# Performance work log

Measured on AMD Instinct MI355X. Metric: run time of the kernel, lower is better.

The kernel has to match this reference:

```python
import jax, jax.numpy as jnp
import numpy as np

B, S, D, H, F, L = 16, 512, 512, 8, 2048, 3  # L layers: 1 in blocks_1 + 2 in blocks_2
DK = D // H
EPS = 1e-5

def setup_inputs():
    key = jax.random.key(0)
    ks = jax.random.split(key, 10)
    sc = 1.0 / np.sqrt(D)
    return dict(
        q_embed_data=jax.random.normal(ks[0], (B, S, D), jnp.float32),
        qa_embed_data=jax.random.normal(ks[1], (B, S, D), jnp.float32),
        Wk=jax.random.normal(ks[2], (L, D, D), jnp.float32) * sc,
        bk=jnp.zeros((L, D), jnp.float32),
        Wv=jax.random.normal(ks[3], (L, D, D), jnp.float32) * sc,
        bv=jnp.zeros((L, D), jnp.float32),
        Wo=jax.random.normal(ks[4], (L, D, D), jnp.float32) * sc,
        bo=jnp.zeros((L, D), jnp.float32),
        gammas=jax.random.normal(ks[5], (L, H, 1, 1), jnp.float32) * 0.5,
        ln1_g=jnp.ones((L, D), jnp.float32),
        ln1_b=jnp.zeros((L, D), jnp.float32),
        W1=jax.random.normal(ks[6], (L, D, F), jnp.float32) * sc,
        b1=jnp.zeros((L, F), jnp.float32),
        W2=jax.random.normal(ks[7], (L, F, D), jnp.float32) * (1.0 / np.sqrt(F)),
        b2=jnp.zeros((L, D), jnp.float32),
        ln2_g=jnp.ones((L, D), jnp.float32),
        ln2_b=jnp.zeros((L, D), jnp.float32),
    )

def _ln(x, g, b):
    m = jnp.mean(x, -1, keepdims=True)
    v = jnp.mean((x - m) ** 2, -1, keepdims=True)
    return (x - m) * jax.lax.rsqrt(v + EPS) * g + b

def _attention(q, k, v, mask, gamma):
    # q,k,v: [B,H,S,DK]; mask: [1,1,S,S] bool; gamma: [H,1,1]
    scores = jnp.einsum('bhid,bhjd->bhij', q, k) / np.sqrt(DK)
    maskf = mask.astype(scores.dtype)
    # first (no-grad in torch) softmax pass for distance decay
    p = jax.nn.softmax(jnp.where(mask, scores, -1e32), axis=-1) * maskf
    distcum = jnp.cumsum(p, axis=-1)
    disttot = jnp.sum(p, axis=-1, keepdims=True)
    idx = jnp.arange(scores.shape[-1])
    pos = jnp.abs(idx[None, :] - idx[:, None]).astype(scores.dtype)[None, None]
    dist = jax.lax.stop_gradient(
        jnp.sqrt(jnp.clip((disttot - distcum) * pos, 0.0, None)))
    g = -jax.nn.softplus(gamma)[None]  # [1,H,1,1]
    total_effect = jnp.clip(jnp.exp(dist * g), 1e-5, 1e5)
    scores = jnp.where(mask, scores * total_effect, -1e32)
    attn = jax.nn.softmax(scores, axis=-1)
    return jnp.einsum('bhij,bhjd->bhid', attn, v)

def _mha(q_in, k_in, v_in, mask, Wk, bk, Wv, bv, Wo, bo, gamma):
    bsz = q_in.shape[0]
    def proj(x, W, b):
        return (x @ W + b).reshape(bsz, -1, H, DK).transpose(0, 2, 1, 3)
    q = proj(q_in, Wk, bk)  # kq_same=True -> q uses k_linear
    k = proj(k_in, Wk, bk)
    v = proj(v_in, Wv, bv)
    o = _attention(q, k, v, mask, gamma)
    o = o.transpose(0, 2, 1, 3).reshape(bsz, -1, D)
    return o @ Wo + bo

def _block(i, mask, query, key, values, apply_pos, P):
    q2 = _mha(query, key, values, mask, P['Wk'][i], P['bk'][i], P['Wv'][i],
              P['bv'][i], P['Wo'][i], P['bo'][i], P['gammas'][i])
    x = _ln(query + q2, P['ln1_g'][i], P['ln1_b'][i])
    if apply_pos:
        h = jax.nn.relu(x @ P['W1'][i] + P['b1'][i]) @ P['W2'][i] + P['b2'][i]
        x = _ln(x + h, P['ln2_g'][i], P['ln2_b'][i])
    return x

def reference(q_embed_data, qa_embed_data, Wk, bk, Wv, bv, Wo, bo, gammas,
              ln1_g, ln1_b, W1, b1, W2, b2, ln2_g, ln2_b):
    P = dict(Wk=Wk, bk=bk, Wv=Wv, bv=bv, Wo=Wo, bo=bo, gammas=gammas,
             ln1_g=ln1_g, ln1_b=ln1_b, W1=W1, b1=b1, W2=W2, b2=b2,
             ln2_g=ln2_g, ln2_b=ln2_b)
    s = q_embed_data.shape[1]
    mask1 = jnp.tril(jnp.ones((s, s), bool))[None, None]        # mask==1: current+past
    mask0 = jnp.tril(jnp.ones((s, s), bool), -1)[None, None]    # mask==0: strictly past
    y = qa_embed_data
    x = q_embed_data
    y = _block(0, mask1, y, y, y, True, P)    # blocks_1: knowledge encoder
    x = _block(1, mask1, x, x, x, False, P)   # blocks_2: question encoder (no FFN)
    x = _block(2, mask0, x, x, y, True, P)    # blocks_2: knowledge retriever
    return x
```

## Files before the change

### kernel.cpp

```cpp
#include <hip/hip_runtime.h>
#include <hip/hip_bf16.h>

#define Bdim 16
#define Sdim 512
#define Ddim 512
#define Hdim 8
#define DKdim 64
#define Fdim 2048
#define Mrows (Bdim * Sdim)

typedef __attribute__((ext_vector_type(8))) short  frag16;
typedef __attribute__((ext_vector_type(4))) float  f32x4;
typedef __attribute__((ext_vector_type(8))) unsigned short ushort8;
typedef __attribute__((ext_vector_type(4))) unsigned short ushort4v;

__device__ __forceinline__ unsigned short f2b(float x) {
    union { float f; unsigned int u; } v; v.f = x;
    unsigned int r = (v.u + 0x7FFFu + ((v.u >> 16) & 1u)) >> 16;
    return (unsigned short)r;
}

__global__ __launch_bounds__(256) void gemm_mfma(
    const __hip_bfloat16* __restrict__ A, const __hip_bfloat16* __restrict__ Bt,
    const float* __restrict__ bias, const float* __restrict__ R,
    float* __restrict__ Cf, unsigned short* __restrict__ Cb,
    int M, int N, int K, int do_relu)
{
    __shared__ short As[2][128 * 32];
    __shared__ short Bs[2][128 * 32];

    const int t = threadIdx.x;
    const int lane = t & 63;
    const int wave = t >> 6;

    const int gx = gridDim.x;
    const int nb = gx * gridDim.y;
    const int lid = blockIdx.x + gx * blockIdx.y;
    const int wid = (lid & 7) * (nb >> 3) + (lid >> 3);
    const int bm = (wid / gx) * 128;
    const int bn = (wid % gx) * 128;

    const int wm = (wave >> 1) * 64;
    const int wn = (wave & 1) * 64;

    f32x4 acc[4][4] = {};
    const int lrow = lane >> 2;
    const int lcol = (lane & 3) * 8;

    auto stage = [&](int k0, int buf) {
#pragma unroll
        for (int i = 0; i < 2; ++i) {
            const int chunk = wave * 2 + i;
            const int row = chunk * 16 + lrow;
            const __hip_bfloat16* ga = A + (size_t)(bm + row) * K + k0 + lcol;
            const __hip_bfloat16* gb = Bt + (size_t)(bn + row) * K + k0 + lcol;
            __builtin_amdgcn_global_load_lds(
                (const __attribute__((address_space(1))) unsigned int*)ga,
                (__attribute__((address_space(3))) unsigned int*)(&As[buf][chunk * 512]),
                16, 0, 0);
            __builtin_amdgcn_global_load_lds(
                (const __attribute__((address_space(1))) unsigned int*)gb,
                (__attribute__((address_space(3))) unsigned int*)(&Bs[buf][chunk * 512]),
                16, 0, 0);
        }
    };

    const int fr = lane & 15;
    const int quad = lane >> 4;
    const int nk = K >> 5;

    stage(0, 0);
    __syncthreads();

    for (int it = 0; it < nk; ++it) {
        const int buf = it & 1;
        if (it + 1 < nk) stage((it + 1) << 5, buf ^ 1);
        frag16 af[4], bfr[4];
#pragma unroll
        for (int i = 0; i < 4; ++i) {
            af[i]  = *(const frag16*)(&As[buf][(wm + i * 16 + fr) * 32 + quad * 8]);
            bfr[i] = *(const frag16*)(&Bs[buf][(wn + i * 16 + fr) * 32 + quad * 8]);
        }
#pragma unroll
        for (int mi = 0; mi < 4; ++mi)
#pragma unroll
            for (int ni = 0; ni < 4; ++ni)
                acc[mi][ni] = __builtin_amdgcn_mfma_f32_16x16x32_bf16(
                    af[mi], bfr[ni], acc[mi][ni], 0, 0, 0);
        __syncthreads();
    }

#pragma unroll
    for (int mi = 0; mi < 4; ++mi) {
#pragma unroll
        for (int r = 0; r < 4; ++r) {
            const int m = bm + wm + mi * 16 + quad * 4 + r;
#pragma unroll
            for (int ni = 0; ni < 4; ++ni) {
                const int n = bn + wn + ni * 16 + fr;
                float v = acc[mi][ni][r] + bias[n];
                if (R) v += R[(size_t)m * N + n];
                if (do_relu) v = fmaxf(v, 0.f);
                if (Cf) Cf[(size_t)m * N + n] = v;
                if (Cb) Cb[(size_t)m * N + n] = f2b(v);
            }
        }
    }
}

__global__ __launch_bounds__(256) void gemm_n64(
    const unsigned short* __restrict__ A0, const unsigned short* __restrict__ A1,
    const unsigned short* __restrict__ B0, const unsigned short* __restrict__ B1,
    const float* __restrict__ bias0, const float* __restrict__ bias1,
    const float* __restrict__ R, float* __restrict__ Cf,
    unsigned short* __restrict__ Cb, unsigned short* __restrict__ CbT,
    int K)
{
    const int NN = 512;
    __shared__ short As[2][128 * 32];
    __shared__ short Bs[2][64 * 32];

    const int trans = blockIdx.z;
    const unsigned short* A  = trans ? A1 : A0;
    const unsigned short* Bt = trans ? B1 : B0;
    const float* bias        = trans ? bias1 : bias0;

    const int t = threadIdx.x;
    const int lane = t & 63;
    const int wave = t >> 6;

    const int lid = blockIdx.x + 8 * blockIdx.y;
    const int wid = (lid & 7) * 64 + (lid >> 3);
    const int bm = (wid >> 3) * 128;
    const int bn = (wid & 7) * 64;

    const int wm = (wave >> 1) * 64;
    const int wn = (wave & 1) * 32;

    f32x4 acc[4][2] = {};
    const int lrow = lane >> 2;
    const int lcol = (lane & 3) * 8;

    auto stage = [&](int k0, int buf) {
#pragma unroll
        for (int i = 0; i < 2; ++i) {
            const int chunk = wave * 2 + i;
            const int row = chunk * 16 + lrow;
            const unsigned short* ga = A + (size_t)(bm + row) * K + k0 + lcol;
            __builtin_amdgcn_global_load_lds(
                (const __attribute__((address_space(1))) unsigned int*)ga,
                (__attribute__((address_space(3))) unsigned int*)(&As[buf][chunk * 512]),
                16, 0, 0);
        }
        {
            const int row = wave * 16 + lrow;
            const unsigned short* gb = Bt + (size_t)(bn + row) * K + k0 + lcol;
            __builtin_amdgcn_global_load_lds(
                (const __attribute__((address_space(1))) unsigned int*)gb,
                (__attribute__((address_space(3))) unsigned int*)(&Bs[buf][wave * 512]),
                16, 0, 0);
        }
    };

    const int fr = lane & 15;
    const int quad = lane >> 4;
    const int nk = K >> 5;

    stage(0, 0);
    __syncthreads();

    for (int it = 0; it < nk; ++it) {
        const int buf = it & 1;
        if (it + 1 < nk) stage((it + 1) << 5, buf ^ 1);
        frag16 af[4], bfr[2];
#pragma unroll
        for (int i = 0; i < 4; ++i)
            af[i] = *(const frag16*)(&As[buf][(wm + i * 16 + fr) * 32 + quad * 8]);
#pragma unroll
        for (int i = 0; i < 2; ++i)
            bfr[i] = *(const frag16*)(&Bs[buf][(wn + i * 16 + fr) * 32 + quad * 8]);
#pragma unroll
        for (int mi = 0; mi < 4; ++mi)
#pragma unroll
            for (int ni = 0; ni < 2; ++ni)
                acc[mi][ni] = __builtin_amdgcn_mfma_f32_16x16x32_bf16(
                    af[mi], bfr[ni], acc[mi][ni], 0, 0, 0);
        __syncthreads();
    }

    if (trans) {
#pragma unroll
        for (int mi = 0; mi < 4; ++mi)
#pragma unroll
            for (int ni = 0; ni < 2; ++ni) {
                const int m = bm + wm + mi * 16 + quad * 4;
                const int n = bn + wn + ni * 16 + fr;
                ushort4v o;
#pragma unroll
                for (int r = 0; r < 4; ++r) o[r] = f2b(acc[mi][ni][r] + bias[n]);
                const int bb = m >> 9, s = m & 511;
                const int hh = n >> 6, dd = n & 63;
                *(ushort4v*)(CbT + (((size_t)((bb * Hdim + hh) * DKdim + dd)) << 9) + s) = o;
            }
        return;
    }

#pragma unroll
    for (int mi = 0; mi < 4; ++mi) {
#pragma unroll
        for (int r = 0; r < 4; ++r) {
            const int m = bm + wm + mi * 16 + quad * 4 + r;
#pragma unroll
            for (int ni = 0; ni < 2; ++ni) {
                const int n = bn + wn + ni * 16 + fr;
                float v = acc[mi][ni][r] + bias[n];
                if (R) v += R[(size_t)m * NN + n];
                if (Cf) Cf[(size_t)m * NN + n] = v;
                if (Cb) Cb[(size_t)m * NN + n] = f2b(v);
            }
        }
    }
}

__global__ __launch_bounds__(256) void conv_b(
    const float* __restrict__ X, unsigned short* __restrict__ Y)
{
    const size_t i = ((size_t)blockIdx.x * 256 + threadIdx.x) * 8;
    float4 a = *(const float4*)(X + i);
    float4 b = *(const float4*)(X + i + 4);
    ushort8 o;
    o[0] = f2b(a.x); o[1] = f2b(a.y); o[2] = f2b(a.z); o[3] = f2b(a.w);
    o[4] = f2b(b.x); o[5] = f2b(b.y); o[6] = f2b(b.z); o[7] = f2b(b.w);
    *(ushort8*)(Y + i) = o;
}

__global__ __launch_bounds__(256) void wtrans_all(
    const float* __restrict__ Wk, const float* __restrict__ Wv,
    const float* __restrict__ Wo, const float* __restrict__ W1,
    const float* __restrict__ W2, unsigned short* __restrict__ dst)
{
    const int bid = blockIdx.x;
    const float* src; unsigned short* d; int K, N, tk, tn;
    if (bid < 576) {
        const int mat = bid >> 6, tile = bid & 63;
        const int l = mat / 3, wch = mat % 3;
        const float* W = (wch == 0) ? Wk : (wch == 1) ? Wv : Wo;
        src = W + (size_t)l * 262144;
        d = dst + (size_t)mat * 262144;
        K = 512; N = 512; tn = tile & 7; tk = tile >> 3;
    } else if (bid < 1088) {
        const int idx = bid - 576, l2 = idx >> 8, tile = idx & 255;
        src = W1 + (size_t)(l2 * 2) * (512 * 2048);
        d = dst + 9 * 262144 + (size_t)l2 * (512 * 2048);
        K = 512; N = 2048; tn = tile & 31; tk = tile >> 5;
    } else {
        const int idx = bid - 1088, l2 = idx >> 8, tile = idx & 255;
        src = W2 + (size_t)(l2 * 2) * (2048 * 512);
        d = dst + 9 * 262144 + 2 * (512 * 2048) + (size_t)l2 * (2048 * 512);
        K = 2048; N = 512; tn = tile & 7; tk = tile >> 3;
    }
    const int n0 = tn * 64, k0 = tk * 64;
    __shared__ float T[64][65];
    const int t = threadIdx.x;
    const int kl = t >> 4, n4 = (t & 15) << 2;
#pragma unroll
    for (int it = 0; it < 4; ++it) {
        const int k = kl + it * 16;
        float4 v = *(const float4*)(src + (size_t)(k0 + k) * N + n0 + n4);
        T[n4 + 0][k] = v.x; T[n4 + 1][k] = v.y;
        T[n4 + 2][k] = v.z; T[n4 + 3][k] = v.w;
    }
    __syncthreads();
    const int nl = t >> 3, k8 = (t & 7) << 3;
#pragma unroll
    for (int it = 0; it < 2; ++it) {
        const int n = nl + it * 32;
        ushort8 o;
#pragma unroll
        for (int c = 0; c < 8; ++c) o[c] = f2b(T[n][k8 + c]);
        *(ushort8*)(d + (size_t)(n0 + n) * K + k0 + k8) = o;
    }
}

__global__ __launch_bounds__(128, 16) void attn_flash6(
    const unsigned short* __restrict__ Kb,
    const unsigned short* __restrict__ Vt,
    const float* __restrict__ gam,
    unsigned short* __restrict__ Ob,
    int mask_type)
{
    __shared__ float CTw[16 * 33];
    __shared__ unsigned short Pst[2][16 * 36];
    __shared__ float S1s[2][16];
    __shared__ float S2s[2][16];
    __shared__ float OaccS[16 * 66];

    const int h = blockIdx.y, b = blockIdx.z;
    const int tile = (blockIdx.x + blockIdx.y + 2 * blockIdx.z) & 31;

    const int t = threadIdx.x, lane = t & 63, p = t >> 6;
    const int quad = lane >> 4, fr = lane & 15;
    const int q0 = tile * 16;
    const int iRow = q0 + fr;

    const unsigned short* kbase = Kb + (size_t)b * Sdim * Ddim + h * DKdim;

    frag16 aq0 = *(const frag16*)(kbase + (size_t)(q0 + fr) * Ddim + quad * 8);
    frag16 aq1 = *(const frag16*)(kbase + (size_t)(q0 + fr) * Ddim + 32 + quad * 8);

    const int jnmax = tile;

    float psum = 0.f;
    for (int jn = p; jn <= jnmax; jn += 2) {
        frag16 k0 = *(const frag16*)(kbase + (size_t)(jn * 16 + fr) * Ddim + quad * 8);
        frag16 k1 = *(const frag16*)(kbase + (size_t)(jn * 16 + fr) * Ddim + 32 + quad * 8);
        f32x4 z = {0.f, 0.f, 0.f, 0.f};
        z = __builtin_amdgcn_mfma_f32_16x16x32_bf16(k0, aq0, z, 0, 0, 0);
        z = __builtin_amdgcn_mfma_f32_16x16x32_bf16(k1, aq1, z, 0, 0, 0);
        const int jbase = jn * 16 + quad * 4;
        float tq = 0.f;
#pragma unroll
        for (int r = 0; r < 4; ++r) {
            const int j = jbase + r;
            const bool valid = mask_type ? (j <= iRow) : (j < iRow);
            tq += valid ? __expf(z[r] * 0.125f) : 0.f;
        }
        psum += tq;
        float tt = tq;
        tt += __shfl_xor(tt, 16);
        tt += __shfl_xor(tt, 32);
        if (quad == 0) CTw[fr * 33 + jn] = tt;
    }
    {
        float s1 = psum;
        s1 += __shfl_xor(s1, 16);
        s1 += __shfl_xor(s1, 32);
        if (lane < 16) S1s[p][lane] = s1;
    }
    __syncthreads();

    if (p == 0 && lane < 16) {
        float run = 0.f;
        for (int jn = 31; jn >= 0; --jn) {
            const float tv = (jn <= jnmax) ? CTw[lane * 33 + jn] : 0.f;
            CTw[lane * 33 + jn] = run;
            run += tv;
        }
    }
    __syncthreads();

    const float rsum1 = 1.f / (S1s[0][fr] + S1s[1][fr]);
    const float gneg = -log1pf(__expf(gam[h]));

    unsigned short* Pw = Pst[p];
    const unsigned short* vtb = Vt + (size_t)(b * Hdim + h) * DKdim * Sdim;
    const bool fm_blk = (mask_type == 0) && (q0 == 0);
    const bool fmrow = (mask_type == 0) && (iRow == 0);
    const int umax = fm_blk ? (Sdim / 32 - 1) : (tile >> 1);
    float sum2p = 0.f;
    f32x4 oacc[4] = {};

    for (int u = umax - p; u >= 0; u -= 2) {
#pragma unroll
        for (int half = 0; half < 2; ++half) {
            const int jn = 2 * u + half;
            frag16 k0 = *(const frag16*)(kbase + (size_t)(jn * 16 + fr) * Ddim + quad * 8);
            frag16 k1 = *(const frag16*)(kbase + (size_t)(jn * 16 + fr) * Ddim + 32 + quad * 8);
            f32x4 z = {0.f, 0.f, 0.f, 0.f};
            z = __builtin_amdgcn_mfma_f32_16x16x32_bf16(k0, aq0, z, 0, 0, 0);
            z = __builtin_amdgcn_mfma_f32_16x16x32_bf16(k1, aq1, z, 0, 0, 0);
            const int jbase = jn * 16 + quad * 4;
            float s[4], e1[4], lsuf[4];
            float tq = 0.f;
#pragma unroll
            for (int r = 3; r >= 0; --r) {
                lsuf[r] = tq;
                const int j = jbase + r;
                const bool valid = mask_type ? (j <= iRow) : (j < iRow);
                s[r] = z[r] * 0.125f;
                e1[r] = valid ? __expf(s[r]) : 0.f;
                tq += e1[r];
            }
            float incl = tq;
            {
                float u1 = __shfl_down(incl, 16);
                incl += (quad < 3) ? u1 : 0.f;
                float u2 = __shfl_down(incl, 32);
                incl += (quad < 2) ? u2 : 0.f;
            }
            const float qsuf = incl - tq;
            const float ct = CTw[fr * 33 + jn];
            ushort4v pk;
#pragma unroll
            for (int r = 0; r < 4; ++r) {
                const int j = jbase + r;
                const bool valid = mask_type ? (j <= iRow) : (j < iRow);
                const float suf = ct + qsuf + lsuf[r];
                const float ratio = suf * rsum1;
                const int dd = iRow - j;
                const float pos = (float)(dd >= 0 ? dd : -dd);
                const float arg = (ratio > 0.f) ? ratio * pos : 0.f;
                const float te = fminf(fmaxf(__expf(gneg * sqrtf(arg)), 1e-5f), 1e5f);
                const float e2 = valid ? __expf(s[r] * te) : (fmrow ? 1.f : 0.f);
                sum2p += e2;
                pk[r] = f2b(e2);
            }
            *(ushort4v*)(Pw + fr * 36 + half * 16 + quad * 4) = pk;
        }
        frag16 pf = *(const frag16*)(Pw + fr * 36 + quad * 8);
        const int jb = u * 32;
#pragma unroll
        for (int dt = 0; dt < 4; ++dt) {
            frag16 vf = *(const frag16*)(vtb + (size_t)(dt * 16 + fr) * Sdim + jb + quad * 8);
            oacc[dt] = __builtin_amdgcn_mfma_f32_16x16x32_bf16(pf, vf, oacc[dt], 0, 0, 0);
        }
    }

    {
        float s2 = sum2p;
        s2 += __shfl_xor(s2, 16);
        s2 += __shfl_xor(s2, 32);
        if (lane < 16) S2s[p][lane] = s2;
    }
    if (p == 1) {
#pragma unroll
        for (int dt = 0; dt < 4; ++dt)
#pragma unroll
            for (int r = 0; r < 4; ++r)
                OaccS[(quad * 4 + r) * 66 + dt * 16 + fr] = oacc[dt][r];
    }
    __syncthreads();

    if (p == 0) {
        const float rs2 = 1.f / (S2s[0][fr] + S2s[1][fr]);
        float rs2q[4];
#pragma unroll
        for (int r = 0; r < 4; ++r) rs2q[r] = __shfl(rs2, quad * 4 + r);

        unsigned short* obase = Ob + ((size_t)(b * Sdim + q0)) * Ddim + h * DKdim;
#pragma unroll
        for (int dt = 0; dt < 4; ++dt)
#pragma unroll
            for (int r = 0; r < 4; ++r) {
                const float v = oacc[dt][r] + OaccS[(quad * 4 + r) * 66 + dt * 16 + fr];
                obase[(size_t)(quad * 4 + r) * Ddim + dt * 16 + fr] = f2b(v * rs2q[r]);
            }
    }
}

__global__ __launch_bounds__(256) void ln_kernel(
    const float* __restrict__ X, const float* __restrict__ g,
    const float* __restrict__ bta, float* __restrict__ Y,
    unsigned short* __restrict__ Yb)
{
    const int row = blockIdx.x;
    const int t = threadIdx.x;
    __shared__ float r1[256], r2[256];
    const float* x = X + (size_t)row * Ddim;
    float a = x[t], b = x[t + 256];
    r1[t] = a + b;
    r2[t] = a * a + b * b;
    __syncthreads();
    for (int off = 128; off; off >>= 1) {
        if (t < off) { r1[t] += r1[t + off]; r2[t] += r2[t + off]; }
        __syncthreads();
    }
    float mean = r1[0] * (1.f / Ddim);
    float var = r2[0] * (1.f / Ddim) - mean * mean;
    float rs = rsqrtf(var + 1e-5f);
    float y0 = (a - mean) * rs * g[t] + bta[t];
    float y1 = (b - mean) * rs * g[t + 256] + bta[t + 256];
    if (Y) {
        float* y = Y + (size_t)row * Ddim;
        y[t] = y0;
        y[t + 256] = y1;
    }
    if (Yb) {
        unsigned short* yb = Yb + (size_t)row * Ddim;
        yb[t] = f2b(y0);
        yb[t + 256] = f2b(y1);
    }
}

extern "C" void kernel_launch(void* const* d_in, const int* in_sizes, int n_in,
                              void* d_out, int out_size, void* d_ws, size_t ws_size,
                              hipStream_t stream)
{
    const float* x0     = (const float*)d_in[0];
    const float* y0     = (const float*)d_in[1];
    const float* Wk     = (const float*)d_in[2];
    const float* bk     = (const float*)d_in[3];
    const float* Wv     = (const float*)d_in[4];
    const float* bv     = (const float*)d_in[5];
    const float* Wo     = (const float*)d_in[6];
    const float* bo     = (const float*)d_in[7];
    const float* gammas = (const float*)d_in[8];
    const float* ln1g   = (const float*)d_in[9];
    const float* ln1b   = (const float*)d_in[10];
    const float* W1     = (const float*)d_in[11];
    const float* b1     = (const float*)d_in[12];
    const float* W2     = (const float*)d_in[13];
    const float* b2     = (const float*)d_in[14];
    const float* ln2g   = (const float*)d_in[15];
    const float* ln2b   = (const float*)d_in[16];

    const size_t NBSD = (size_t)Mrows * Ddim;
    float* ws = (float*)d_ws;
    float* T1   = ws;
    float* X1   = T1 + NBSD;
    float* Xbuf = X1 + NBSD;
    unsigned short* Kbf = (unsigned short*)(Xbuf + NBSD);
    unsigned short* Vt  = Kbf + NBSD;
    unsigned short* AOb = Vt + NBSD;
    unsigned short* Abf = AOb + NBSD;
    unsigned short* Xbf = Abf + NBSD;
    unsigned short* Ybf = Xbf + NBSD;
    unsigned short* Hbb = Ybf + NBSD;
    unsigned short* WtAll = Hbb + (size_t)Mrows * Fdim;

    auto WtK = [&](int l) { return WtAll + (size_t)(l * 3 + 0) * 262144; };
    auto WtV = [&](int l) { return WtAll + (size_t)(l * 3 + 1) * 262144; };
    auto WtO = [&](int l) { return WtAll + (size_t)(l * 3 + 2) * 262144; };
    auto Wt1 = [&](int l) { return WtAll + 9 * 262144 + (size_t)(l >> 1) * (512 * 2048); };
    auto Wt2 = [&](int l) { return WtAll + 9 * 262144 + 2 * (512 * 2048) + (size_t)(l >> 1) * (2048 * 512); };

    const int convBlocks = (int)(NBSD / 2048);

    wtrans_all<<<1600, 256, 0, stream>>>(Wk, Wv, Wo, W1, W2, WtAll);

    auto run_block = [&](int l, const float* qinf, const unsigned short* qinb,
                         const unsigned short* vinb, int mask_type, bool ffn,
                         float* outf, unsigned short* outb) {
        const float* bk_l = bk + (size_t)l * Ddim;
        const float* bv_l = bv + (size_t)l * Ddim;
        const float* bo_l = bo + (size_t)l * Ddim;

        gemm_n64<<<dim3(8, 64, 2), 256, 0, stream>>>(
            qinb, vinb, WtK(l), WtV(l), bk_l, bv_l,
            nullptr, nullptr, Kbf, Vt, Ddim);
        attn_flash6<<<dim3(Sdim / 16, Hdim, Bdim), 128, 0, stream>>>(
            Kbf, Vt, gammas + (size_t)l * Hdim, AOb, mask_type);
        gemm_n64<<<dim3(8, 64, 1), 256, 0, stream>>>(
            AOb, AOb, WtO(l), WtO(l), bo_l, bo_l,
            qinf, T1, nullptr, nullptr, Ddim);
        float* x1f = ffn ? X1 : outf;
        unsigned short* x1b = ffn ? Abf : outb;
        ln_kernel<<<Mrows, 256, 0, stream>>>(T1,
            ln1g + (size_t)l * Ddim, ln1b + (size_t)l * Ddim, x1f, x1b);
        if (ffn) {
            const float* b1_l = b1 + (size_t)l * Fdim;
            const float* b2_l = b2 + (size_t)l * Ddim;
            gemm_mfma<<<dim3(Fdim / 128, Mrows / 128), 256, 0, stream>>>(
                (const __hip_bfloat16*)Abf, (const __hip_bfloat16*)Wt1(l),
                b1_l, nullptr, nullptr, Hbb, Mrows, Fdim, Ddim, 1);
            gemm_n64<<<dim3(8, 64, 1), 256, 0, stream>>>(
                Hbb, Hbb, Wt2(l), Wt2(l), b2_l, b2_l,
                X1, T1, nullptr, nullptr, Fdim);
            ln_kernel<<<Mrows, 256, 0, stream>>>(T1,
                ln2g + (size_t)l * Ddim, ln2b + (size_t)l * Ddim, outf, outb);
        }
    };

    conv_b<<<convBlocks, 256, 0, stream>>>(y0, Abf);
    run_block(0, y0, Abf, Abf, 1, true, nullptr, Ybf);
    conv_b<<<convBlocks, 256, 0, stream>>>(x0, Abf);
    run_block(1, x0, Abf, Abf, 1, false, Xbuf, Xbf);
    run_block(2, Xbuf, Xbf, Ybf, 0, true, (float*)d_out, nullptr);
}
```

Before: 665.7 us.

## Pair causal attention tiles per block and trim masked and exp work

Each attention block now handles two query tiles (i and 31-i), so every block does a similar amount of causal work and the grid shrinks to 16 blocks in x. Inside the kernel, exponentials switch to exp2 with pre-scaled constants. Per-element mask tests run only on diagonal tiles. Fully masked key tiles skip the QK MFMA and write constant probabilities instead. The upper clamp on the decay factor is dropped, and the bf16 packing uses a paired conversion intrinsic. In exchange there are fewer blocks in flight, a longer serial loop per block, and a looser launch-bounds occupancy hint.

```diff
diff --git a/kernel.cpp b/kernel.cpp
--- a/kernel.cpp
+++ b/kernel.cpp
@@ -13,6 +13,16 @@
 typedef __attribute__((ext_vector_type(4))) float  f32x4;
 typedef __attribute__((ext_vector_type(8))) unsigned short ushort8;
 typedef __attribute__((ext_vector_type(4))) unsigned short ushort4v;
+
+#if defined(__has_builtin)
+#  if __has_builtin(__builtin_amdgcn_exp2f)
+#    define EXP2(x) __builtin_amdgcn_exp2f(x)
+#  endif
+#endif
+#ifndef EXP2
+#  define EXP2(x) __expf((x) * 0.6931471805599453f)
+#endif
+#define SC2 0.18033688011112042f
 
 __device__ __forceinline__ unsigned short f2b(float x) {
     union { float f; unsigned int u; } v; v.f = x;
@@ -282,7 +292,7 @@
     }
 }
 
-__global__ __launch_bounds__(128, 16) void attn_flash6(
+__global__ __launch_bounds__(128, 4) void attn_flash7(
     const unsigned short* __restrict__ Kb,
     const unsigned short* __restrict__ Vt,
     const float* __restrict__ gam,
@@ -296,155 +306,172 @@
     __shared__ float OaccS[16 * 66];
 
     const int h = blockIdx.y, b = blockIdx.z;
-    const int tile = (blockIdx.x + blockIdx.y + 2 * blockIdx.z) & 31;
-
     const int t = threadIdx.x, lane = t & 63, p = t >> 6;
     const int quad = lane >> 4, fr = lane & 15;
-    const int q0 = tile * 16;
-    const int iRow = q0 + fr;
 
     const unsigned short* kbase = Kb + (size_t)b * Sdim * Ddim + h * DKdim;
-
-    frag16 aq0 = *(const frag16*)(kbase + (size_t)(q0 + fr) * Ddim + quad * 8);
-    frag16 aq1 = *(const frag16*)(kbase + (size_t)(q0 + fr) * Ddim + 32 + quad * 8);
-
-    const int jnmax = tile;
-
-    float psum = 0.f;
-    for (int jn = p; jn <= jnmax; jn += 2) {
-        frag16 k0 = *(const frag16*)(kbase + (size_t)(jn * 16 + fr) * Ddim + quad * 8);
-        frag16 k1 = *(const frag16*)(kbase + (size_t)(jn * 16 + fr) * Ddim + 32 + quad * 8);
-        f32x4 z = {0.f, 0.f, 0.f, 0.f};
-        z = __builtin_amdgcn_mfma_f32_16x16x32_bf16(k0, aq0, z, 0, 0, 0);
-        z = __builtin_amdgcn_mfma_f32_16x16x32_bf16(k1, aq1, z, 0, 0, 0);
-        const int jbase = jn * 16 + quad * 4;
-        float tq = 0.f;
-#pragma unroll
-        for (int r = 0; r < 4; ++r) {
-            const int j = jbase + r;
-            const bool valid = mask_type ? (j <= iRow) : (j < iRow);
-            tq += valid ? __expf(z[r] * 0.125f) : 0.f;
-        }
-        psum += tq;
-        float tt = tq;
-        tt += __shfl_xor(tt, 16);
-        tt += __shfl_xor(tt, 32);
-        if (quad == 0) CTw[fr * 33 + jn] = tt;
-    }
-    {
-        float s1 = psum;
-        s1 += __shfl_xor(s1, 16);
-        s1 += __shfl_xor(s1, 32);
-        if (lane < 16) S1s[p][lane] = s1;
-    }
-    __syncthreads();
-
-    if (p == 0 && lane < 16) {
-        float run = 0.f;
-        for (int jn = 31; jn >= 0; --jn) {
-            const float tv = (jn <= jnmax) ? CTw[lane * 33 + jn] : 0.f;
-            CTw[lane * 33 + jn] = run;
-            run += tv;
-        }
-    }
-    __syncthreads();
-
-    const float rsum1 = 1.f / (S1s[0][fr] + S1s[1][fr]);
-    const float gneg = -log1pf(__expf(gam[h]));
-
-    unsigned short* Pw = Pst[p];
     const unsigned short* vtb = Vt + (size_t)(b * Hdim + h) * DKdim * Sdim;
-    const bool fm_blk = (mask_type == 0) && (q0 == 0);
-    const bool fmrow = (mask_type == 0) && (iRow == 0);
-    const int umax = fm_blk ? (Sdim / 32 - 1) : (tile >> 1);
-    float sum2p = 0.f;
-    f32x4 oacc[4] = {};
-
-    for (int u = umax - p; u >= 0; u -= 2) {
-#pragma unroll
-        for (int half = 0; half < 2; ++half) {
-            const int jn = 2 * u + half;
+    const float gneg2 = -log1pf(__expf(gam[h])) * 1.4426950408889634f;
+
+    for (int half_t = 0; half_t < 2; ++half_t) {
+        const int tile = half_t ? (31 - blockIdx.x) : blockIdx.x;
+        const int q0 = tile * 16;
+        const int iRow = q0 + fr;
+
+        frag16 aq0 = *(const frag16*)(kbase + (size_t)(q0 + fr) * Ddim + quad * 8);
+        frag16 aq1 = *(const frag16*)(kbase + (size_t)(q0 + fr) * Ddim + 32 + quad * 8);
+
+        float psum = 0.f;
+        for (int jn = p; jn <= tile; jn += 2) {
             frag16 k0 = *(const frag16*)(kbase + (size_t)(jn * 16 + fr) * Ddim + quad * 8);
             frag16 k1 = *(const frag16*)(kbase + (size_t)(jn * 16 + fr) * Ddim + 32 + quad * 8);
             f32x4 z = {0.f, 0.f, 0.f, 0.f};
             z = __builtin_amdgcn_mfma_f32_16x16x32_bf16(k0, aq0, z, 0, 0, 0);
             z = __builtin_amdgcn_mfma_f32_16x16x32_bf16(k1, aq1, z, 0, 0, 0);
-            const int jbase = jn * 16 + quad * 4;
-            float s[4], e1[4], lsuf[4];
             float tq = 0.f;
-#pragma unroll
-            for (int r = 3; r >= 0; --r) {
-                lsuf[r] = tq;
-                const int j = jbase + r;
-                const bool valid = mask_type ? (j <= iRow) : (j < iRow);
-                s[r] = z[r] * 0.125f;
-                e1[r] = valid ? __expf(s[r]) : 0.f;
-                tq += e1[r];
-            }
-            float incl = tq;
-            {
-                float u1 = __shfl_down(incl, 16);
-                incl += (quad < 3) ? u1 : 0.f;
-                float u2 = __shfl_down(incl, 32);
-                incl += (quad < 2) ? u2 : 0.f;
-            }
-            const float qsuf = incl - tq;
-            const float ct = CTw[fr * 33 + jn];
-            ushort4v pk;
-#pragma unroll
-            for (int r = 0; r < 4; ++r) {
-                const int j = jbase + r;
-                const bool valid = mask_type ? (j <= iRow) : (j < iRow);
-                const float suf = ct + qsuf + lsuf[r];
-                const float ratio = suf * rsum1;
-                const int dd = iRow - j;
-                const float pos = (float)(dd >= 0 ? dd : -dd);
-                const float arg = (ratio > 0.f) ? ratio * pos : 0.f;
-                const float te = fminf(fmaxf(__expf(gneg * sqrtf(arg)), 1e-5f), 1e5f);
-                const float e2 = valid ? __expf(s[r] * te) : (fmrow ? 1.f : 0.f);
-                sum2p += e2;
-                pk[r] = f2b(e2);
-            }
-            *(ushort4v*)(Pw + fr * 36 + half * 16 + quad * 4) = pk;
-        }
-        frag16 pf = *(const frag16*)(Pw + fr * 36 + quad * 8);
-        const int jb = u * 32;
-#pragma unroll
-        for (int dt = 0; dt < 4; ++dt) {
-            frag16 vf = *(const frag16*)(vtb + (size_t)(dt * 16 + fr) * Sdim + jb + quad * 8);
-            oacc[dt] = __builtin_amdgcn_mfma_f32_16x16x32_bf16(pf, vf, oacc[dt], 0, 0, 0);
-        }
-    }
-
-    {
-        float s2 = sum2p;
-        s2 += __shfl_xor(s2, 16);
-        s2 += __shfl_xor(s2, 32);
-        if (lane < 16) S2s[p][lane] = s2;
-    }
-    if (p == 1) {
-#pragma unroll
-        for (int dt = 0; dt < 4; ++dt)
-#pragma unroll
-            for (int r = 0; r < 4; ++r)
-                OaccS[(quad * 4 + r) * 66 + dt * 16 + fr] = oacc[dt][r];
-    }
-    __syncthreads();
-
-    if (p == 0) {
-        const float rs2 = 1.f / (S2s[0][fr] + S2s[1][fr]);
-        float rs2q[4];
-#pragma unroll
-        for (int r = 0; r < 4; ++r) rs2q[r] = __shfl(rs2, quad * 4 + r);
-
-        unsigned short* obase = Ob + ((size_t)(b * Sdim + q0)) * Ddim + h * DKdim;
-#pragma unroll
-        for (int dt = 0; dt < 4; ++dt)
-#pragma unroll
-            for (int r = 0; r < 4; ++r) {
-                const float v = oacc[dt][r] + OaccS[(quad * 4 + r) * 66 + dt * 16 + fr];
-                obase[(size_t)(quad * 4 + r) * Ddim + dt * 16 + fr] = f2b(v * rs2q[r]);
-            }
+            if (jn < tile) {
+#pragma unroll
+                for (int r = 0; r < 4; ++r) tq += EXP2(z[r] * SC2);
+            } else {
+#pragma unroll
+                for (int r = 0; r < 4; ++r) {
+                    const bool valid = mask_type ? (quad * 4 + r <= fr)
+                                                 : (quad * 4 + r < fr);
+                    tq += valid ? EXP2(z[r] * SC2) : 0.f;
+                }
+            }
+            psum += tq;
+            float tt = tq;
+            tt += __shfl_xor(tt, 16);
+            tt += __shfl_xor(tt, 32);
+            if (quad == 0) CTw[fr * 33 + jn] = tt;
+        }
+        {
+            float s1 = psum;
+            s1 += __shfl_xor(s1, 16);
+            s1 += __shfl_xor(s1, 32);
+            if (lane < 16) S1s[p][lane] = s1;
+        }
+        __syncthreads();
+
+        if (p == 0 && lane < 16) {
+            float run = 0.f;
+            for (int jn = tile; jn >= 0; --jn) {
+                const float tv = CTw[lane * 33 + jn];
+                CTw[lane * 33 + jn] = run;
+                run += tv;
+            }
+        }
+        __syncthreads();
+
+        const float rsum1 = 1.f / (S1s[0][fr] + S1s[1][fr]);
+        unsigned short* Pw = Pst[p];
+        const bool fm_blk = (mask_type == 0) && (tile == 0);
+        const bool fmrow = fm_blk && (fr == 0);
+        const int umax = fm_blk ? (Sdim / 32 - 1) : (tile >> 1);
+        float sum2p = 0.f;
+        f32x4 oacc[4] = {};
+
+        for (int u = umax - p; u >= 0; u -= 2) {
+#pragma unroll
+            for (int half = 0; half < 2; ++half) {
+                const int jn = 2 * u + half;
+                uint2 pku;
+                if (jn > tile) {
+                    const unsigned int pv = fmrow ? 0x3F803F80u : 0u;
+                    pku.x = pv; pku.y = pv;
+                    sum2p += fmrow ? 4.f : 0.f;
+                } else {
+                    frag16 k0 = *(const frag16*)(kbase + (size_t)(jn * 16 + fr) * Ddim + quad * 8);
+                    frag16 k1 = *(const frag16*)(kbase + (size_t)(jn * 16 + fr) * Ddim + 32 + quad * 8);
+                    f32x4 z = {0.f, 0.f, 0.f, 0.f};
+                    z = __builtin_amdgcn_mfma_f32_16x16x32_bf16(k0, aq0, z, 0, 0, 0);
+                    z = __builtin_amdgcn_mfma_f32_16x16x32_bf16(k1, aq1, z, 0, 0, 0);
+                    const bool full = (jn < tile);
+                    float s2r[4], lsuf[4];
+                    float tq = 0.f;
+#pragma unroll
+                    for (int r = 3; r >= 0; --r) {
+                        lsuf[r] = tq;
+                        s2r[r] = z[r] * SC2;
+                        float e1 = EXP2(s2r[r]);
+                        if (!full) {
+                            const bool valid = mask_type ? (quad * 4 + r <= fr)
+                                                         : (quad * 4 + r < fr);
+                            e1 = valid ? e1 : 0.f;
+                        }
+                        tq += e1;
+                    }
+                    float incl = tq;
+                    {
+                        float u1 = __shfl_down(incl, 16);
+                        incl += (quad < 3) ? u1 : 0.f;
+                        float u2 = __shfl_down(incl, 32);
+                        incl += (quad < 2) ? u2 : 0.f;
+                    }
+                    const float base = CTw[fr * 33 + jn] + (incl - tq);
+                    const float pos0 = (float)(iRow - (jn * 16 + quad * 4));
+                    float e2v[4];
+#pragma unroll
+                    for (int r = 0; r < 4; ++r) {
+                        const float ratio = (base + lsuf[r]) * rsum1;
+                        const float arg = ratio * fabsf(pos0 - (float)r);
+                        const float te = fmaxf(EXP2(gneg2 * sqrtf(arg)), 1e-5f);
+                        float e2 = EXP2(s2r[r] * te);
+                        if (!full) {
+                            const bool valid = mask_type ? (quad * 4 + r <= fr)
+                                                         : (quad * 4 + r < fr);
+                            e2 = valid ? e2 : (fmrow ? 1.f : 0.f);
+                        }
+                        sum2p += e2;
+                        e2v[r] = e2;
+                    }
+                    union { __hip_bfloat162 hh; unsigned int u; } c0, c1;
+                    c0.hh = __float22bfloat162_rn(make_float2(e2v[0], e2v[1]));
+                    c1.hh = __float22bfloat162_rn(make_float2(e2v[2], e2v[3]));
+                    pku.x = c0.u; pku.y = c1.u;
+                }
+                *(uint2*)(Pw + fr * 36 + half * 16 + quad * 4) = pku;
+            }
+            frag16 pf = *(const frag16*)(Pw + fr * 36 + quad * 8);
+            const int jb = u * 32;
+#pragma unroll
+            for (int dt = 0; dt < 4; ++dt) {
+                frag16 vf = *(const frag16*)(vtb + (size_t)(dt * 16 + fr) * Sdim + jb + quad * 8);
+                oacc[dt] = __builtin_amdgcn_mfma_f32_16x16x32_bf16(pf, vf, oacc[dt], 0, 0, 0);
+            }
+        }
+
+        {
+            float s2 = sum2p;
+            s2 += __shfl_xor(s2, 16);
+            s2 += __shfl_xor(s2, 32);
+            if (lane < 16) S2s[p][lane] = s2;
+        }
+        if (p == 1) {
+#pragma unroll
+            for (int dt = 0; dt < 4; ++dt)
+#pragma unroll
+                for (int r = 0; r < 4; ++r)
+                    OaccS[(quad * 4 + r) * 66 + dt * 16 + fr] = oacc[dt][r];
+        }
+        __syncthreads();
+
+        if (p == 0) {
+            const float rs2 = 1.f / (S2s[0][fr] + S2s[1][fr]);
+            float rs2q[4];
+#pragma unroll
+            for (int r = 0; r < 4; ++r) rs2q[r] = __shfl(rs2, quad * 4 + r);
+
+            unsigned short* obase = Ob + ((size_t)(b * Sdim + q0)) * Ddim + h * DKdim;
+#pragma unroll
+            for (int dt = 0; dt < 4; ++dt)
+#pragma unroll
+                for (int r = 0; r < 4; ++r) {
+                    const float v = oacc[dt][r] + OaccS[(quad * 4 + r) * 66 + dt * 16 + fr];
+                    obase[(size_t)(quad * 4 + r) * Ddim + dt * 16 + fr] = f2b(v * rs2q[r]);
+                }
+        }
     }
 }
 
@@ -538,7 +565,7 @@
         gemm_n64<<<dim3(8, 64, 2), 256, 0, stream>>>(
             qinb, vinb, WtK(l), WtV(l), bk_l, bv_l,
             nullptr, nullptr, Kbf, Vt, Ddim);
-        attn_flash6<<<dim3(Sdim / 16, Hdim, Bdim), 128, 0, stream>>>(
+        attn_flash7<<<dim3(16, Hdim, Bdim), 128, 0, stream>>>(
             Kbf, Vt, gammas + (size_t)l * Hdim, AOb, mask_type);
         gemm_n64<<<dim3(8, 64, 1), 256, 0, stream>>>(
             AOb, AOb, WtO(l), WtO(l), bo_l, bo_l,
```

Result: faster. 646.4 us (-2.9%).
